# Kernel optimization log

Hardware: AMD Instinct MI355X
Metric: run time of the kernel (lower is better)

## Reference

```python
import jax, jax.numpy as jnp
import numpy as np

N_NODES = 100000
N_EDGES = 1600000
D_IN = 128
D_HID = 128
D_OUT = 128


def setup_inputs() -> dict:
    key = jax.random.key(0)
    ks = jax.random.split(key, 9)
    x = jax.random.normal(ks[0], (N_NODES, D_IN), dtype=jnp.float32)
    src = jax.random.randint(ks[1], (N_EDGES,), 0, N_NODES, dtype=jnp.int32)
    dst = jax.random.randint(ks[2], (N_EDGES,), 0, N_NODES, dtype=jnp.int32)
    s = 1.0 / np.sqrt(D_IN)
    Wc = jax.random.uniform(ks[3], (D_IN, D_HID), dtype=jnp.float32, minval=-s, maxval=s)
    bc = jnp.zeros((D_HID,), dtype=jnp.float32)
    s1 = 1.0 / np.sqrt(D_HID)
    W1 = jax.random.uniform(ks[4], (D_HID, D_HID), dtype=jnp.float32, minval=-s1, maxval=s1)
    b1 = jax.random.uniform(ks[5], (D_HID,), dtype=jnp.float32, minval=-s1, maxval=s1)
    W2 = jax.random.uniform(ks[6], (D_HID, D_OUT), dtype=jnp.float32, minval=-s1, maxval=s1)
    b2 = jax.random.uniform(ks[7], (D_OUT,), dtype=jnp.float32, minval=-s1, maxval=s1)
    return {"x": x, "src": src, "dst": dst, "Wc": Wc, "bc": bc,
            "W1": W1, "b1": b1, "W2": W2, "b2": b2}


def reference(x, src, dst, Wc, bc, W1, b1, W2, b2):
    # DGL GraphConv with norm='both' (default), no edge_weight:
    #   h = x / sqrt(out_deg(src));  agg[v] = sum_{(u->v)} h[u];  agg /= sqrt(in_deg(v))
    ones = jnp.ones((src.shape[0],), dtype=x.dtype)
    deg_out = jax.ops.segment_sum(ones, src, num_segments=N_NODES)
    deg_in = jax.ops.segment_sum(ones, dst, num_segments=N_NODES)
    norm_out = jax.lax.rsqrt(jnp.clip(deg_out, 1.0))[:, None]  # [N,1]
    norm_in = jax.lax.rsqrt(jnp.clip(deg_in, 1.0))[:, None]

    h = x * norm_out
    msgs = h[src]                                              # [E, D_in]
    agg = jax.ops.segment_sum(msgs, dst, num_segments=N_NODES) # [N, D_in]
    agg = agg * norm_in
    h = agg @ Wc + bc                                          # GraphConv linear

    # num_layers == 2 path: relu -> fc -> relu -> fc2
    h = jax.nn.relu(h)
    h = h @ W1 + b1
    h = jax.nn.relu(h)
    out = h @ W2 + b2
    return out
```

## Files before the change

kernel.cpp:

```cpp
#include <hip/hip_runtime.h>
#include <hip/hip_fp16.h>

#define NN 100000
#define NE 1600000
#define NBK 782
#define MAXB 2560
#define EPB 4096
#define NPB 391

typedef __attribute__((ext_vector_type(8))) _Float16 f16x8;
typedef __attribute__((ext_vector_type(4))) _Float16 f16x4;
typedef __attribute__((ext_vector_type(4))) float f32x4;

__global__ __launch_bounds__(256) void phase1_kernel(const int* __restrict__ src,
                                                     const int* __restrict__ dst,
                                                     int* __restrict__ cursorA,
                                                     int* __restrict__ cursorO,
                                                     int* __restrict__ tempA,
                                                     unsigned char* __restrict__ tempO8) {
    __shared__ int cntA[NBK], cntO[NBK];
    const int t = threadIdx.x;
    for (int b = t; b < NBK; b += 256) { cntA[b] = 0; cntO[b] = 0; }
    __syncthreads();
    const int e0 = blockIdx.x * EPB;
    int rD[16], rS[16];
#pragma unroll
    for (int i = 0; i < 16; ++i) {
        int e = e0 + i * 256 + t;
        if (e < NE) {
            rD[i] = atomicAdd(&cntA[dst[e] >> 7], 1);
            rS[i] = atomicAdd(&cntO[src[e] >> 7], 1);
        }
    }
    __syncthreads();
    for (int b = t; b < NBK; b += 256) {
        int c = cntA[b];
        cntA[b] = c ? (b * MAXB + atomicAdd(&cursorA[b], c)) : 0;
        c = cntO[b];
        cntO[b] = c ? (b * MAXB + atomicAdd(&cursorO[b], c)) : 0;
    }
    __syncthreads();
#pragma unroll
    for (int i = 0; i < 16; ++i) {
        int e = e0 + i * 256 + t;
        if (e < NE) {
            int d = dst[e], s = src[e];
            tempA[cntA[d >> 7] + rD[i]] = ((d & 127) << 17) | s;
            tempO8[cntO[s >> 7] + rS[i]] = (unsigned char)(s & 127);
        }
    }
}

__global__ __launch_bounds__(256) void phase2_kernel(const int* __restrict__ cursorA,
                                                     const int* __restrict__ cursorO,
                                                     const int* __restrict__ tempA,
                                                     const unsigned char* __restrict__ tempO8,
                                                     const float* __restrict__ x,
                                                     int* __restrict__ csr_src,
                                                     int2* __restrict__ rowext,
                                                     __half* __restrict__ xh) {
    __shared__ int buf[MAXB];
    __shared__ int cnt[128], ex[128], run[128], cntO[128];
    const int b = blockIdx.x;
    const int t = threadIdx.x;
    const int cA = cursorA[b];
    const int cO = cursorO[b];
    const int base = b * MAXB;
    if (t < 128) { cnt[t] = 0; cntO[t] = 0; run[t] = 0; }
    __syncthreads();
    for (int i = t; i < cA; i += 256) {
        int w = tempA[base + i];
        buf[i] = w;
        atomicAdd(&cnt[(w >> 17) & 127], 1);
    }
    for (int i = t; i < cO; i += 256)
        atomicAdd(&cntO[tempO8[base + i]], 1);
    __syncthreads();
    {
        int r = t >> 1;
        int node = b * 128 + r;
        if (node < NN) {
            float nO = rsqrtf(fmaxf((float)cntO[r], 1.0f));
            int c0 = (t & 1) * 64;
#pragma unroll
            for (int i = 0; i < 16; ++i) {
                float4 v = *reinterpret_cast<const float4*>(&x[(size_t)node * 128 + c0 + i * 4]);
                __half2 h01 = __floats2half2_rn(v.x * nO, v.y * nO);
                __half2 h23 = __floats2half2_rn(v.z * nO, v.w * nO);
                __half2 hh[2] = {h01, h23};
                *reinterpret_cast<float2*>(&xh[(size_t)node * 128 + c0 + i * 4]) =
                    *reinterpret_cast<float2*>(hh);
            }
        }
    }
    if (t < 128) ex[t] = cnt[t];
    __syncthreads();
    for (int o = 1; o < 128; o <<= 1) {
        int u = (t >= o && t < 128) ? ex[t - o] : 0;
        __syncthreads();
        if (t < 128) ex[t] += u;
        __syncthreads();
    }
    if (t < 128) {
        int node = b * 128 + t;
        if (node < NN)
            rowext[node] = make_int2(base + ex[t] - cnt[t], base + ex[t]);
    }
    __syncthreads();
    for (int i = t; i < cA; i += 256) {
        int w = buf[i];
        int n = (w >> 17) & 127;
        int r = atomicAdd(&run[n], 1);
        csr_src[base + ex[n] - cnt[n] + r] = w & 0x1FFFF;
    }
}

__global__ __launch_bounds__(256) void gather_kernel(const __half* __restrict__ xh,
                                                     const int2* __restrict__ rowext,
                                                     const int* __restrict__ csr_src,
                                                     __half* __restrict__ aggh) {
    int node = blockIdx.x * 8 + (threadIdx.x >> 5);
    int lane = threadIdx.x & 31;
    if (node >= NN) return;
    int2 be = rowext[node];
    int beg = be.x, end = be.y;
    float ax = 0.f, ay = 0.f, az = 0.f, aw = 0.f;
    int j = beg;
    for (; j + 4 <= end; j += 4) {
        int s0 = csr_src[j], s1 = csr_src[j + 1], s2 = csr_src[j + 2], s3 = csr_src[j + 3];
        float2 r0 = *reinterpret_cast<const float2*>(&xh[(size_t)s0 * 128 + lane * 4]);
        float2 r1 = *reinterpret_cast<const float2*>(&xh[(size_t)s1 * 128 + lane * 4]);
        float2 r2 = *reinterpret_cast<const float2*>(&xh[(size_t)s2 * 128 + lane * 4]);
        float2 r3 = *reinterpret_cast<const float2*>(&xh[(size_t)s3 * 128 + lane * 4]);
        const __half2* p0 = reinterpret_cast<const __half2*>(&r0);
        const __half2* p1 = reinterpret_cast<const __half2*>(&r1);
        const __half2* p2 = reinterpret_cast<const __half2*>(&r2);
        const __half2* p3 = reinterpret_cast<const __half2*>(&r3);
        float2 l0 = __half22float2(p0[0]), h0 = __half22float2(p0[1]);
        float2 l1 = __half22float2(p1[0]), h1 = __half22float2(p1[1]);
        float2 l2 = __half22float2(p2[0]), h2 = __half22float2(p2[1]);
        float2 l3 = __half22float2(p3[0]), h3 = __half22float2(p3[1]);
        ax += l0.x + l1.x + l2.x + l3.x;
        ay += l0.y + l1.y + l2.y + l3.y;
        az += h0.x + h1.x + h2.x + h3.x;
        aw += h0.y + h1.y + h2.y + h3.y;
    }
    for (; j < end; ++j) {
        int s = csr_src[j];
        float2 r = *reinterpret_cast<const float2*>(&xh[(size_t)s * 128 + lane * 4]);
        const __half2* p = reinterpret_cast<const __half2*>(&r);
        float2 l = __half22float2(p[0]), h = __half22float2(p[1]);
        ax += l.x; ay += l.y; az += h.x; aw += h.y;
    }
    float ni = rsqrtf(fmaxf((float)(end - beg), 1.0f));
    __half2 o01 = __floats2half2_rn(ax * ni, ay * ni);
    __half2 o23 = __floats2half2_rn(az * ni, aw * ni);
    __half2 oo[2] = {o01, o23};
    *reinterpret_cast<float2*>(&aggh[(size_t)node * 256 + lane * 4]) =
        *reinterpret_cast<float2*>(oo);
}

__global__ __launch_bounds__(256) void wprep_kernel(const float* __restrict__ Wc,
                                                    const float* __restrict__ W1,
                                                    const float* __restrict__ W2,
                                                    _Float16* __restrict__ Wf) {
    int t = blockIdx.x * 256 + threadIdx.x;
    if (t >= 3 * 4 * 8 * 64) return;
    int lane = t & 63;
    int ct = (t >> 6) & 7;
    int kt = (t >> 9) & 3;
    int layer = t >> 11;
    const float* W = (layer == 0) ? Wc : (layer == 1) ? W1 : W2;
    int c = ct * 16 + (lane & 15);
    int kbase = kt * 32 + (lane >> 4) * 8;
    f16x8 v;
#pragma unroll
    for (int j = 0; j < 8; ++j)
        v[j] = (_Float16)W[(size_t)(kbase + j) * 128 + c];
    reinterpret_cast<f16x8*>(Wf)[t] = v;
}

struct MlpState {
    f32x4 acc[8];
    float bv[3][8];
};

#define ISSUE_CHUNK(G, SLOT)                                                    \
    {                                                                           \
        _Pragma("unroll") for (int i = 0; i < 2; ++i) {                         \
            int s = wv * 2 + i;                                                 \
            size_t goff = ((size_t)((G)*8 + s)) * 1024 + (size_t)lane * 16;     \
            __builtin_amdgcn_global_load_lds(                                   \
                (const __attribute__((address_space(1))) unsigned int*)(Wb + goff), \
                (__attribute__((address_space(3))) unsigned int*)(&WL[SLOT][s * 1024]), \
                16, 0, 0);                                                      \
        }                                                                       \
    }

template <int C>
__device__ __forceinline__ void mstep(const char* __restrict__ Wb,
                                      char (&WL)[5][8192],
                                      _Float16 (&HS)[64][136],
                                      MlpState& st,
                                      float* __restrict__ Cout, int n, int row0,
                                      int lane, int wv, int mrow, int kg) {
    constexpr int layer = C >> 2;
    constexpr int kt = C & 3;
    constexpr int VM = (C <= 8) ? 6 : 2 * (11 - C);

    asm volatile("s_waitcnt vmcnt(%0)" ::"i"(VM) : "memory");
    __builtin_amdgcn_s_barrier();

    if constexpr (C + 4 < 12) {
        ISSUE_CHUNK(C + 4, (C + 4) % 5)
    }

    if constexpr (kt == 0) {
#pragma unroll
        for (int i = 0; i < 8; ++i) st.acc[i] = (f32x4){0.f, 0.f, 0.f, 0.f};
    }
    f16x8 a = *reinterpret_cast<const f16x8*>(&HS[wv * 16 + mrow][kt * 32 + kg * 8]);

#pragma unroll
    for (int ct = 0; ct < 8; ++ct) {
        f16x8 w = *reinterpret_cast<const f16x8*>(&WL[C % 5][(ct * 64 + lane) * 16]);
        st.acc[ct] = __builtin_amdgcn_mfma_f32_16x16x32_f16(a, w, st.acc[ct], 0, 0, 0);
    }

    if constexpr (kt == 3) {
        if constexpr (layer < 2) {
#pragma unroll
            for (int ct = 0; ct < 8; ++ct)
#pragma unroll
                for (int r = 0; r < 4; ++r)
                    HS[wv * 16 + kg * 4 + r][ct * 16 + mrow] =
                        (_Float16)fmaxf(st.acc[ct][r] + st.bv[layer][ct], 0.f);
            asm volatile("s_waitcnt lgkmcnt(0)" ::: "memory");
        } else {
#pragma unroll
            for (int ct = 0; ct < 8; ++ct)
#pragma unroll
                for (int r = 0; r < 4; ++r) {
                    int grow = row0 + wv * 16 + kg * 4 + r;
                    if (grow < n)
                        Cout[(size_t)grow * 128 + ct * 16 + mrow] = st.acc[ct][r] + st.bv[2][ct];
                }
        }
    }
}

__global__ __launch_bounds__(256, 2) void mlp_mfma(const __half* __restrict__ Ah,
                                                   const _Float16* __restrict__ Wf,
                                                   const float* __restrict__ bc,
                                                   const float* __restrict__ b1,
                                                   const float* __restrict__ b2,
                                                   float* __restrict__ C, int n) {
    __shared__ _Float16 HS[64][136];
    __shared__ char WL[5][8192];
    const int tid = threadIdx.x;
    const int lane = tid & 63;
    const int wv = tid >> 6;
    const int row0 = blockIdx.x * 64;
    const int mrow = lane & 15;
    const int kg = lane >> 4;
    const char* Wb = (const char*)Wf;

    ISSUE_CHUNK(0, 0)
    ISSUE_CHUNK(1, 1)
    ISSUE_CHUNK(2, 2)
    ISSUE_CHUNK(3, 3)

    {
        int r = tid >> 5;
        int c4 = (tid & 31) * 4;
#pragma unroll
        for (int i = 0; i < 8; ++i) {
            int row = i * 8 + r;
            int grow = row0 + row;
            f16x4 hv = (f16x4){(_Float16)0.f, (_Float16)0.f, (_Float16)0.f, (_Float16)0.f};
            if (grow < n)
                hv = *reinterpret_cast<const f16x4*>(&Ah[(size_t)grow * 256 + c4]);
            *reinterpret_cast<f16x4*>(&HS[row][c4]) = hv;
        }
    }
    MlpState st;
#pragma unroll
    for (int ct = 0; ct < 8; ++ct) {
        st.bv[0][ct] = bc[ct * 16 + mrow];
        st.bv[1][ct] = b1[ct * 16 + mrow];
        st.bv[2][ct] = b2[ct * 16 + mrow];
    }
    __syncthreads();

    mstep<0>(Wb, WL, HS, st, C, n, row0, lane, wv, mrow, kg);
    mstep<1>(Wb, WL, HS, st, C, n, row0, lane, wv, mrow, kg);
    mstep<2>(Wb, WL, HS, st, C, n, row0, lane, wv, mrow, kg);
    mstep<3>(Wb, WL, HS, st, C, n, row0, lane, wv, mrow, kg);
    mstep<4>(Wb, WL, HS, st, C, n, row0, lane, wv, mrow, kg);
    mstep<5>(Wb, WL, HS, st, C, n, row0, lane, wv, mrow, kg);
    mstep<6>(Wb, WL, HS, st, C, n, row0, lane, wv, mrow, kg);
    mstep<7>(Wb, WL, HS, st, C, n, row0, lane, wv, mrow, kg);
    mstep<8>(Wb, WL, HS, st, C, n, row0, lane, wv, mrow, kg);
    mstep<9>(Wb, WL, HS, st, C, n, row0, lane, wv, mrow, kg);
    mstep<10>(Wb, WL, HS, st, C, n, row0, lane, wv, mrow, kg);
    mstep<11>(Wb, WL, HS, st, C, n, row0, lane, wv, mrow, kg);
}

extern "C" void kernel_launch(void* const* d_in, const int* in_sizes, int n_in,
                              void* d_out, int out_size, void* d_ws, size_t ws_size,
                              hipStream_t stream) {
    const float* x  = (const float*)d_in[0];
    const int*  src = (const int*)d_in[1];
    const int*  dst = (const int*)d_in[2];
    const float* Wc = (const float*)d_in[3];
    const float* bc = (const float*)d_in[4];
    const float* W1 = (const float*)d_in[5];
    const float* b1 = (const float*)d_in[6];
    const float* W2 = (const float*)d_in[7];
    const float* b2 = (const float*)d_in[8];
    float* out = (float*)d_out;
    __half* aggh = (__half*)d_out;

    char* p = (char*)d_ws;
    _Float16* Wf = (_Float16*)p;        p += 196608;
    __half* xh = (__half*)p;            p += (size_t)NN * 128 * 2;
    int* tempA = (int*)p;               p += (size_t)NBK * MAXB * 4;
    unsigned char* tempO8 = (unsigned char*)p; p += (size_t)NBK * MAXB;
    int* cursorA  = (int*)p;            p += (size_t)NBK * 4;
    int* cursorO  = (int*)p;            p += (size_t)NBK * 4;
    int2* rowext  = (int2*)p;           p += (size_t)NN * 8;
    int* csr_src  = (int*)p;

    wprep_kernel<<<24, 256, 0, stream>>>(Wc, W1, W2, Wf);
    hipMemsetAsync(cursorA, 0, (size_t)2 * NBK * sizeof(int), stream);
    phase1_kernel<<<NPB, 256, 0, stream>>>(src, dst, cursorA, cursorO, tempA, tempO8);
    phase2_kernel<<<NBK, 256, 0, stream>>>(cursorA, cursorO, tempA, tempO8,
                                           x, csr_src, rowext, xh);

    gather_kernel<<<(NN + 7) / 8, 256, 0, stream>>>(xh, rowext, csr_src, aggh);

    mlp_mfma<<<(NN + 63) / 64, 256, 0, stream>>>(aggh, Wf, bc, b1, b2, out, NN);
}
```

Before: 187.7 us.

## Stage bucketed edges in LDS for coalesced scatter in phase1

The bucketing kernel now handles twice as many edges per block. It computes local bucket offsets with a block-wide prefix scan, then locally sorts edges into shared memory by bucket before writing them to the global temp arrays. This turns scattered per-edge global writes into mostly contiguous runs per bucket. In exchange it adds several barriers and scans, uses much more LDS (which may reduce occupancy), re-reads src/dst, and halves the number of blocks.

```diff
diff --git a/kernel.cpp b/kernel.cpp
--- a/kernel.cpp
+++ b/kernel.cpp
@@ -5,8 +5,8 @@
 #define NE 1600000
 #define NBK 782
 #define MAXB 2560
-#define EPB 4096
-#define NPB 391
+#define EPB 8192
+#define NPB 196
 
 typedef __attribute__((ext_vector_type(8))) _Float16 f16x8;
 typedef __attribute__((ext_vector_type(4))) _Float16 f16x4;
@@ -18,36 +18,99 @@
                                                      int* __restrict__ cursorO,
                                                      int* __restrict__ tempA,
                                                      unsigned char* __restrict__ tempO8) {
-    __shared__ int cntA[NBK], cntO[NBK];
+    __shared__ int cntA[1024];
+    __shared__ int cntO[1024];
+    __shared__ int gofsA[NBK];
+    __shared__ int gofsO[NBK];
+    __shared__ int runA[NBK];
+    __shared__ int scanT[256];
+    __shared__ int edgeBuf[EPB];
+    __shared__ unsigned short bkt16[EPB];
+
     const int t = threadIdx.x;
-    for (int b = t; b < NBK; b += 256) { cntA[b] = 0; cntO[b] = 0; }
-    __syncthreads();
     const int e0 = blockIdx.x * EPB;
-    int rD[16], rS[16];
-#pragma unroll
-    for (int i = 0; i < 16; ++i) {
-        int e = e0 + i * 256 + t;
-        if (e < NE) {
-            rD[i] = atomicAdd(&cntA[dst[e] >> 7], 1);
-            rS[i] = atomicAdd(&cntO[src[e] >> 7], 1);
-        }
-    }
-    __syncthreads();
+    const int nE = min(EPB, NE - e0);
+
+    for (int i = t; i < 1024; i += 256) { cntA[i] = 0; cntO[i] = 0; }
+    __syncthreads();
+    for (int i = t; i < nE; i += 256) {
+        atomicAdd(&cntA[dst[e0 + i] >> 7], 1);
+        atomicAdd(&cntO[src[e0 + i] >> 7], 1);
+    }
+    __syncthreads();
+
+    int a[4], sA = 0;
+#pragma unroll
+    for (int k = 0; k < 4; ++k) { a[k] = cntA[4 * t + k]; sA += a[k]; }
+    scanT[t] = sA;
+    __syncthreads();
+    for (int o = 1; o < 256; o <<= 1) {
+        int u = (t >= o) ? scanT[t - o] : 0;
+        __syncthreads();
+        scanT[t] += u;
+        __syncthreads();
+    }
+    {
+        int r = scanT[t] - sA;
+#pragma unroll
+        for (int k = 0; k < 4; ++k) { int c = a[k]; cntA[4 * t + k] = r; r += c; }
+    }
+    __syncthreads();
+    int o4[4], sO = 0;
+#pragma unroll
+    for (int k = 0; k < 4; ++k) { o4[k] = cntO[4 * t + k]; sO += o4[k]; }
+    scanT[t] = sO;
+    __syncthreads();
+    for (int o = 1; o < 256; o <<= 1) {
+        int u = (t >= o) ? scanT[t - o] : 0;
+        __syncthreads();
+        scanT[t] += u;
+        __syncthreads();
+    }
+    {
+        int r = scanT[t] - sO;
+#pragma unroll
+        for (int k = 0; k < 4; ++k) { int c = o4[k]; cntO[4 * t + k] = r; r += c; }
+    }
+    __syncthreads();
+
     for (int b = t; b < NBK; b += 256) {
-        int c = cntA[b];
-        cntA[b] = c ? (b * MAXB + atomicAdd(&cursorA[b], c)) : 0;
-        c = cntO[b];
-        cntO[b] = c ? (b * MAXB + atomicAdd(&cursorO[b], c)) : 0;
-    }
-    __syncthreads();
-#pragma unroll
-    for (int i = 0; i < 16; ++i) {
-        int e = e0 + i * 256 + t;
-        if (e < NE) {
-            int d = dst[e], s = src[e];
-            tempA[cntA[d >> 7] + rD[i]] = ((d & 127) << 17) | s;
-            tempO8[cntO[s >> 7] + rS[i]] = (unsigned char)(s & 127);
-        }
+        int ex = cntA[b], c = cntA[b + 1] - ex;
+        gofsA[b] = c ? (b * MAXB + atomicAdd(&cursorA[b], c) - ex) : 0;
+        int exo = cntO[b], co = cntO[b + 1] - exo;
+        gofsO[b] = co ? (b * MAXB + atomicAdd(&cursorO[b], co) - exo) : 0;
+        runA[b] = 0;
+    }
+    __syncthreads();
+
+    for (int i = t; i < nE; i += 256) {
+        int d = dst[e0 + i], s = src[e0 + i];
+        int b = d >> 7;
+        int pos = cntA[b] + atomicAdd(&runA[b], 1);
+        edgeBuf[pos] = ((d & 127) << 17) | s;
+        bkt16[pos] = (unsigned short)b;
+    }
+    __syncthreads();
+    for (int i = t; i < nE; i += 256) {
+        int b = bkt16[i];
+        tempA[gofsA[b] + i] = edgeBuf[i];
+    }
+    __syncthreads();
+    for (int b = t; b < NBK; b += 256) runA[b] = 0;
+    __syncthreads();
+
+    unsigned char* byteBuf = (unsigned char*)edgeBuf;
+    for (int i = t; i < nE; i += 256) {
+        int s = src[e0 + i];
+        int b = s >> 7;
+        int pos = cntO[b] + atomicAdd(&runA[b], 1);
+        byteBuf[pos] = (unsigned char)(s & 127);
+        bkt16[pos] = (unsigned short)b;
+    }
+    __syncthreads();
+    for (int i = t; i < nE; i += 256) {
+        int b = bkt16[i];
+        tempO8[gofsO[b] + i] = byteBuf[i];
     }
 }
 
```

Measured after the change: 179.1 us. 4.6% less time.
